# Kernel tuning notes

Measured on AMD Instinct MI355X. Metric: run time of the kernel, lower is better.

## Reference

```python
import jax, jax.numpy as jnp
import numpy as np

NORM_P = 2  # p-norm used in the original module (self._norm)

def setup_inputs() -> dict:
    key = jax.random.key(0)
    k1, k2 = jax.random.split(key)
    lab_vecs = jax.random.normal(k1, (512, 512), dtype=jnp.float32)   # (M, D) label/order embeddings
    vis_vecs = jax.random.normal(k2, (1024, 512), dtype=jnp.float32)  # (N, D) visual embeddings
    return {"lab_vecs": lab_vecs, "vis_vecs": vis_vecs}

def reference(lab_vecs, vis_vecs):
    # Original: for each visual vector i, score[i, j] = -|| ReLU(lab[j] - vis[i]) ||_p
    # Vectorized over all (N, M) pairs in one broadcasted pass.
    diff = jax.nn.relu(lab_vecs[None, :, :] - vis_vecs[:, None, :])  # (N, M, D)
    if NORM_P == 2:
        order_dis = jnp.sqrt(jnp.sum(diff * diff, axis=-1))          # (N, M)
    else:
        order_dis = jnp.sum(diff ** NORM_P, axis=-1) ** (1.0 / NORM_P)
    return -order_dis
```

## Files before the change

### kernel.cpp

```cpp
#include <hip/hip_runtime.h>
#include <math.h>


typedef float f32x4 __attribute__((ext_vector_type(4)));
typedef float f32x2 __attribute__((ext_vector_type(2)));

#define N_VIS  1024
#define M_LAB  512
#define DDIM   512
#define BK     128
#define NSPLIT 4
#define SLICE  (N_VIS * M_LAB)
#define SURD   66

__global__ __launch_bounds__(256, 2) void order_sim_main_f32(
    const float* __restrict__ lab, const float* __restrict__ vis,
    float* __restrict__ part) {
  __shared__ f32x2 sV[64 * SURD];
  __shared__ f32x2 sL[64 * SURD];

  const int bx = blockIdx.x;
  const int by = blockIdx.y;
  const int bz = blockIdx.z;
  const int t  = threadIdx.x;

  {
    const int row = t >> 2;
    const int c4  = t & 3;
    const float* vb = vis + (size_t)(bx * 64 + row) * DDIM + bz * BK;
    const float* lb = lab + (size_t)(by * 64 + row) * DDIM + bz * BK;
#pragma unroll
    for (int it = 0; it < 8; ++it) {
      const int f4 = c4 + it * 4;
      const int k0 = f4 * 2;
      f32x4 v = *(const f32x4*)(vb + f4 * 4);
      sV[k0 * SURD + row]       = (f32x2){v.x, v.y};
      sV[(k0 + 1) * SURD + row] = (f32x2){v.z, v.w};
      f32x4 l = *(const f32x4*)(lb + f4 * 4);
      sL[k0 * SURD + row]       = (f32x2){l.x, l.y};
      sL[(k0 + 1) * SURD + row] = (f32x2){l.z, l.w};
    }
  }
  __syncthreads();

  const int i0 = (t & 15) * 4;
  const int j0 = (t >> 4) * 4;

  f32x2 acc[4][4];
#pragma unroll
  for (int a = 0; a < 4; ++a)
#pragma unroll
    for (int b = 0; b < 4; ++b) acc[a][b] = (f32x2){0.0f, 0.0f};

  const f32x2 z2 = {0.0f, 0.0f};

#pragma unroll 4
  for (int k = 0; k < BK / 2; ++k) {
    const f32x2* pv = sV + k * SURD;
    const f32x2* pl = sL + k * SURD;
    f32x4 aA = *(const f32x4*)(pv + i0);
    f32x4 aB = *(const f32x4*)(pv + i0 + 2);
    f32x4 bA = *(const f32x4*)(pl + j0);
    f32x4 bB = *(const f32x4*)(pl + j0 + 2);
    f32x2 a[4], b[4];
    a[0] = (f32x2){aA.x, aA.y};
    a[1] = (f32x2){aA.z, aA.w};
    a[2] = (f32x2){aB.x, aB.y};
    a[3] = (f32x2){aB.z, aB.w};
    b[0] = (f32x2){bA.x, bA.y};
    b[1] = (f32x2){bA.z, bA.w};
    b[2] = (f32x2){bB.x, bB.y};
    b[3] = (f32x2){bB.z, bB.w};
#pragma unroll
    for (int ii = 0; ii < 4; ++ii) {
#pragma unroll
      for (int jj = 0; jj < 4; ++jj) {
        f32x2 d = b[jj] - a[ii];
        d = __builtin_elementwise_max(d, z2);
        acc[ii][jj] = __builtin_elementwise_fma(d, d, acc[ii][jj]);
      }
    }
  }

  float* pw = part + (size_t)bz * SLICE;
#pragma unroll
  for (int ii = 0; ii < 4; ++ii) {
    f32x4 r;
#pragma unroll
    for (int jj = 0; jj < 4; ++jj) {
      f32x2 s = acc[ii][jj];
      r[jj] = s.x + s.y;
    }
    *(f32x4*)(pw + (size_t)(bx * 64 + i0 + ii) * M_LAB + by * 64 + j0) = r;
  }
}

__global__ __launch_bounds__(256) void order_sim_combine(
    const float* __restrict__ part, float* __restrict__ out) {
  const size_t idx = ((size_t)blockIdx.x * 256 + threadIdx.x) * 4;
  f32x4 s = *(const f32x4*)(part + idx);
  s += *(const f32x4*)(part + SLICE + idx);
  s += *(const f32x4*)(part + 2 * (size_t)SLICE + idx);
  s += *(const f32x4*)(part + 3 * (size_t)SLICE + idx);
  f32x4 r;
  r.x = -sqrtf(s.x);
  r.y = -sqrtf(s.y);
  r.z = -sqrtf(s.z);
  r.w = -sqrtf(s.w);
  *(f32x4*)(out + idx) = r;
}

__global__ __launch_bounds__(256) void order_sim_naive(
    const float* __restrict__ lab, const float* __restrict__ vis,
    float* __restrict__ out) {
  const int idx = blockIdx.x * 256 + threadIdx.x;
  const int i = idx >> 9;
  const int j = idx & 511;
  const float* v = vis + (size_t)i * DDIM;
  const float* l = lab + (size_t)j * DDIM;
  float s = 0.0f;
  for (int d = 0; d < DDIM; ++d) {
    float diff = l[d] - v[d];
    diff = fmaxf(diff, 0.0f);
    s = fmaf(diff, diff, s);
  }
  out[idx] = -sqrtf(s);
}

extern "C" void kernel_launch(void* const* d_in, const int* in_sizes, int n_in,
                              void* d_out, int out_size, void* d_ws, size_t ws_size,
                              hipStream_t stream) {
  const float* lab;
  const float* vis;
  if (in_sizes[0] == M_LAB * DDIM) {
    lab = (const float*)d_in[0];
    vis = (const float*)d_in[1];
  } else {
    vis = (const float*)d_in[0];
    lab = (const float*)d_in[1];
  }
  float* out = (float*)d_out;

  const size_t ws_needed = (size_t)NSPLIT * SLICE * sizeof(float);
  if (ws_size >= ws_needed) {
    float* part = (float*)d_ws;
    dim3 grid(N_VIS / 64, M_LAB / 64, NSPLIT);
    order_sim_main_f32<<<grid, 256, 0, stream>>>(lab, vis, part);
    order_sim_combine<<<SLICE / (256 * 4), 256, 0, stream>>>(part, out);
  } else {
    order_sim_naive<<<(N_VIS * M_LAB) / 256, 256, 0, stream>>>(lab, vis, out);
  }
}
```

Baseline: 79.81 us.

## Fuse split-K partials and combine into single kernel with smaller tiles

Replaces the two-kernel split-K scheme with one kernel. Each block loops over all four K chunks in shared memory and applies the sqrt and negation directly, so the workspace round trip and the second launch go away. Block tiles shrink from 64x64 to 32x32 and per-thread tiles from 4x4 to 2x2, which keeps the grid at 512 blocks. In exchange, each LDS load feeds fewer arithmetic operations, and each block now runs a serial chunk loop with barriers and no overlap of global loads.

After: 77.18 us. 3.3% less time.

```diff
diff --git a/kernel.cpp b/kernel.cpp
--- a/kernel.cpp
+++ b/kernel.cpp
@@ -5,126 +5,89 @@
 typedef float f32x4 __attribute__((ext_vector_type(4)));
 typedef float f32x2 __attribute__((ext_vector_type(2)));
 
-#define N_VIS  1024
-#define M_LAB  512
-#define DDIM   512
-#define BK     128
-#define NSPLIT 4
-#define SLICE  (N_VIS * M_LAB)
-#define SURD   66
+#define N_VIS 1024
+#define M_LAB 512
+#define DDIM  512
+#define BK    128
+#define NCH   4
+#define TI    32
+#define TJ    32
+#define SURD  34
 
-__global__ __launch_bounds__(256, 2) void order_sim_main_f32(
+__global__ __launch_bounds__(256, 2) void order_sim_fused(
     const float* __restrict__ lab, const float* __restrict__ vis,
-    float* __restrict__ part) {
+    float* __restrict__ out) {
   __shared__ f32x2 sV[64 * SURD];
   __shared__ f32x2 sL[64 * SURD];
 
   const int bx = blockIdx.x;
   const int by = blockIdx.y;
-  const int bz = blockIdx.z;
   const int t  = threadIdx.x;
 
-  {
-    const int row = t >> 2;
-    const int c4  = t & 3;
-    const float* vb = vis + (size_t)(bx * 64 + row) * DDIM + bz * BK;
-    const float* lb = lab + (size_t)(by * 64 + row) * DDIM + bz * BK;
+  const int i0 = (t & 15) * 2;
+  const int j0 = (t >> 4) * 2;
+
+  const int srow = t >> 3;
+  const int sc8  = t & 7;
+
+  f32x2 acc[2][2];
 #pragma unroll
-    for (int it = 0; it < 8; ++it) {
-      const int f4 = c4 + it * 4;
-      const int k0 = f4 * 2;
-      f32x4 v = *(const f32x4*)(vb + f4 * 4);
-      sV[k0 * SURD + row]       = (f32x2){v.x, v.y};
-      sV[(k0 + 1) * SURD + row] = (f32x2){v.z, v.w};
-      f32x4 l = *(const f32x4*)(lb + f4 * 4);
-      sL[k0 * SURD + row]       = (f32x2){l.x, l.y};
-      sL[(k0 + 1) * SURD + row] = (f32x2){l.z, l.w};
-    }
-  }
-  __syncthreads();
-
-  const int i0 = (t & 15) * 4;
-  const int j0 = (t >> 4) * 4;
-
-  f32x2 acc[4][4];
+  for (int a = 0; a < 2; ++a)
 #pragma unroll
-  for (int a = 0; a < 4; ++a)
-#pragma unroll
-    for (int b = 0; b < 4; ++b) acc[a][b] = (f32x2){0.0f, 0.0f};
+    for (int b = 0; b < 2; ++b) acc[a][b] = (f32x2){0.0f, 0.0f};
 
   const f32x2 z2 = {0.0f, 0.0f};
 
-#pragma unroll 4
-  for (int k = 0; k < BK / 2; ++k) {
-    const f32x2* pv = sV + k * SURD;
-    const f32x2* pl = sL + k * SURD;
-    f32x4 aA = *(const f32x4*)(pv + i0);
-    f32x4 aB = *(const f32x4*)(pv + i0 + 2);
-    f32x4 bA = *(const f32x4*)(pl + j0);
-    f32x4 bB = *(const f32x4*)(pl + j0 + 2);
-    f32x2 a[4], b[4];
-    a[0] = (f32x2){aA.x, aA.y};
-    a[1] = (f32x2){aA.z, aA.w};
-    a[2] = (f32x2){aB.x, aB.y};
-    a[3] = (f32x2){aB.z, aB.w};
-    b[0] = (f32x2){bA.x, bA.y};
-    b[1] = (f32x2){bA.z, bA.w};
-    b[2] = (f32x2){bB.x, bB.y};
-    b[3] = (f32x2){bB.z, bB.w};
+  const float* vbase = vis + (size_t)(bx * TI + srow) * DDIM;
+  const float* lbase = lab + (size_t)(by * TJ + srow) * DDIM;
+
+#pragma unroll 1
+  for (int ch = 0; ch < NCH; ++ch) {
+    if (ch) __syncthreads();
+
+    const float* vb = vbase + ch * BK;
+    const float* lb = lbase + ch * BK;
 #pragma unroll
-    for (int ii = 0; ii < 4; ++ii) {
-#pragma unroll
-      for (int jj = 0; jj < 4; ++jj) {
-        f32x2 d = b[jj] - a[ii];
-        d = __builtin_elementwise_max(d, z2);
-        acc[ii][jj] = __builtin_elementwise_fma(d, d, acc[ii][jj]);
-      }
+    for (int it = 0; it < 4; ++it) {
+      const int f4 = sc8 + it * 8;
+      const int k0 = f4 * 2;
+      f32x4 v = *(const f32x4*)(vb + f4 * 4);
+      sV[k0 * SURD + srow]       = (f32x2){v.x, v.y};
+      sV[(k0 + 1) * SURD + srow] = (f32x2){v.z, v.w};
+      f32x4 l = *(const f32x4*)(lb + f4 * 4);
+      sL[k0 * SURD + srow]       = (f32x2){l.x, l.y};
+      sL[(k0 + 1) * SURD + srow] = (f32x2){l.z, l.w};
+    }
+    __syncthreads();
+
+#pragma unroll 8
+    for (int k = 0; k < BK / 2; ++k) {
+      f32x4 araw = *(const f32x4*)&sV[k * SURD + i0];
+      f32x4 braw = *(const f32x4*)&sL[k * SURD + j0];
+      f32x2 a0 = {araw.x, araw.y};
+      f32x2 a1 = {araw.z, araw.w};
+      f32x2 b0 = {braw.x, braw.y};
+      f32x2 b1 = {braw.z, braw.w};
+
+      f32x2 d;
+      d = b0 - a0; d = __builtin_elementwise_max(d, z2);
+      acc[0][0] = __builtin_elementwise_fma(d, d, acc[0][0]);
+      d = b1 - a0; d = __builtin_elementwise_max(d, z2);
+      acc[0][1] = __builtin_elementwise_fma(d, d, acc[0][1]);
+      d = b0 - a1; d = __builtin_elementwise_max(d, z2);
+      acc[1][0] = __builtin_elementwise_fma(d, d, acc[1][0]);
+      d = b1 - a1; d = __builtin_elementwise_max(d, z2);
+      acc[1][1] = __builtin_elementwise_fma(d, d, acc[1][1]);
     }
   }
 
-  float* pw = part + (size_t)bz * SLICE;
 #pragma unroll
-  for (int ii = 0; ii < 4; ++ii) {
-    f32x4 r;
-#pragma unroll
-    for (int jj = 0; jj < 4; ++jj) {
-      f32x2 s = acc[ii][jj];
-      r[jj] = s.x + s.y;
-    }
-    *(f32x4*)(pw + (size_t)(bx * 64 + i0 + ii) * M_LAB + by * 64 + j0) = r;
+  for (int ii = 0; ii < 2; ++ii) {
+    f32x2 r;
+    r.x = -sqrtf(acc[ii][0].x + acc[ii][0].y);
+    r.y = -sqrtf(acc[ii][1].x + acc[ii][1].y);
+    *(f32x2*)(out + (size_t)(bx * TI + i0 + ii) * M_LAB + by * TJ + j0) = r;
   }
-}
-
-__global__ __launch_bounds__(256) void order_sim_combine(
-    const float* __restrict__ part, float* __restrict__ out) {
-  const size_t idx = ((size_t)blockIdx.x * 256 + threadIdx.x) * 4;
-  f32x4 s = *(const f32x4*)(part + idx);
-  s += *(const f32x4*)(part + SLICE + idx);
-  s += *(const f32x4*)(part + 2 * (size_t)SLICE + idx);
-  s += *(const f32x4*)(part + 3 * (size_t)SLICE + idx);
-  f32x4 r;
-  r.x = -sqrtf(s.x);
-  r.y = -sqrtf(s.y);
-  r.z = -sqrtf(s.z);
-  r.w = -sqrtf(s.w);
-  *(f32x4*)(out + idx) = r;
-}
-
-__global__ __launch_bounds__(256) void order_sim_naive(
-    const float* __restrict__ lab, const float* __restrict__ vis,
-    float* __restrict__ out) {
-  const int idx = blockIdx.x * 256 + threadIdx.x;
-  const int i = idx >> 9;
-  const int j = idx & 511;
-  const float* v = vis + (size_t)i * DDIM;
-  const float* l = lab + (size_t)j * DDIM;
-  float s = 0.0f;
-  for (int d = 0; d < DDIM; ++d) {
-    float diff = l[d] - v[d];
-    diff = fmaxf(diff, 0.0f);
-    s = fmaf(diff, diff, s);
-  }
-  out[idx] = -sqrtf(s);
 }
 
 extern "C" void kernel_launch(void* const* d_in, const int* in_sizes, int n_in,
@@ -141,13 +104,7 @@
   }
   float* out = (float*)d_out;
 
-  const size_t ws_needed = (size_t)NSPLIT * SLICE * sizeof(float);
-  if (ws_size >= ws_needed) {
-    float* part = (float*)d_ws;
-    dim3 grid(N_VIS / 64, M_LAB / 64, NSPLIT);
-    order_sim_main_f32<<<grid, 256, 0, stream>>>(lab, vis, part);
-    order_sim_combine<<<SLICE / (256 * 4), 256, 0, stream>>>(part, out);
-  } else {
-    order_sim_naive<<<(N_VIS * M_LAB) / 256, 256, 0, stream>>>(lab, vis, out);
-  }
+  dim3 grid(N_VIS / TI, M_LAB / TJ);
+  order_sim_fused<<<grid, 256, 0, stream>>>(lab, vis, out);
+  (void)d_ws; (void)ws_size; (void)n_in; (void)out_size;
 }
```
